# Kernel tuning notes

Hardware: AMD Instinct MI355X
Metric: run time of the kernel (lower is better)

The kernel has to match this reference:

```python
import jax, jax.numpy as jnp
import numpy as np

B, T, E, H = 64, 256, 300, 512        # batch, longest_sequence, embed dim, hidden
V, NTAGS, NCLS, DFF = 50000, 17, 18, 256  # vocab, universal POS tags, output classes, dense hidden


def setup_inputs() -> dict:
    key = jax.random.key(0)
    ks = jax.random.split(key, 11)
    su = 1.0 / np.sqrt(H)  # PyTorch LSTMCell/Linear uniform init scale
    return {
        "tokens": jax.random.randint(ks[0], (B, T), 0, V),
        "tags": jax.random.randint(ks[1], (T,), 0, NTAGS),
        "emb": jax.random.normal(ks[2], (V, E), jnp.float32),
        "W_ih": jax.random.uniform(ks[3], (NTAGS, 4 * H, E), jnp.float32, -su, su),
        "W_hh": jax.random.uniform(ks[4], (NTAGS, 4 * H, H), jnp.float32, -su, su),
        "b_ih": jax.random.uniform(ks[5], (NTAGS, 4 * H), jnp.float32, -su, su),
        "b_hh": jax.random.uniform(ks[6], (NTAGS, 4 * H), jnp.float32, -su, su),
        "W1": jax.random.uniform(ks[7], (DFF, H), jnp.float32, -su, su),
        "b1": jax.random.uniform(ks[8], (DFF,), jnp.float32, -su, su),
        "W2": jax.random.uniform(ks[9], (NCLS, DFF), jnp.float32, -1.0 / np.sqrt(DFF), 1.0 / np.sqrt(DFF)),
        "b2": jax.random.uniform(ks[10], (NCLS,), jnp.float32, -1.0 / np.sqrt(DFF), 1.0 / np.sqrt(DFF)),
    }


def reference(tokens, tags, emb, W_ih, W_hh, b_ih, b_hh, W1, b1, W2, b2):
    x = emb[tokens]                     # [B, T, E] embedding lookup
    xs = jnp.swapaxes(x, 0, 1)          # [T, B, E] time-major for scan

    def step(carry, inp):
        h, c = carry
        xt, tag = inp                   # xt: [B, E], tag: scalar int routing the cell
        gates = (xt @ W_ih[tag].T + h @ W_hh[tag].T
                 + b_ih[tag] + b_hh[tag])            # [B, 4H]
        i, f, g, o = jnp.split(gates, 4, axis=-1)    # PyTorch LSTMCell gate order
        i = jax.nn.sigmoid(i)
        f = jax.nn.sigmoid(f)
        g = jnp.tanh(g)
        o = jax.nn.sigmoid(o)
        c = f * c + i * g
        h = o * jnp.tanh(c)
        return (h, c), None

    h0 = jnp.zeros((x.shape[0], H), x.dtype)
    (h, _), _ = jax.lax.scan(step, (h0, h0), (xs, tags))
    # dense head: Linear -> ReLU -> (Dropout inactive at eval) -> Linear
    hid = jax.nn.relu(h @ W1.T + b1)
    return hid @ W2.T + b2              # [B, NCLS] multiclass logits
```

## Files before the change

kernel.cpp:

```cpp
#include <hip/hip_runtime.h>
#include <cstdint>
#include <cstddef>

#define BB   64
#define TT   256
#define EE   300
#define HH   512
#define G4H  2048
#define NCLS 18
#define DFF  256
#define NBLK 128

typedef short short8 __attribute__((ext_vector_type(8)));
typedef float f32x4  __attribute__((ext_vector_type(4)));

__device__ __forceinline__ float fast_exp2(float x) { return __builtin_amdgcn_exp2f(x); }
__device__ __forceinline__ float sigmoid_f(float x) {
  return 1.0f / (1.0f + fast_exp2(x * -1.442695040888963f));
}
__device__ __forceinline__ float tanh_f(float x) {
  return 2.0f / (1.0f + fast_exp2(x * -2.885390081777927f)) - 1.0f;
}
__device__ __forceinline__ unsigned bf16_rne(float x) {
  unsigned u = __float_as_uint(x);
  return (u + 0x7FFFu + ((u >> 16) & 1u)) >> 16;
}
__device__ __forceinline__ float bf16_f32(unsigned hi) { return __uint_as_float(hi << 16); }

__global__ __launch_bounds__(256) void xproj_kernel(
    const int* __restrict__ tokens, const int* __restrict__ tags,
    const float* __restrict__ emb, const float* __restrict__ W_ih,
    const float* __restrict__ b_ih, const float* __restrict__ b_hh,
    float* __restrict__ xW, int t0)
{
  const int tid  = threadIdx.x;
  const int lane = tid & 63;
  const int w    = tid >> 6;
  const int rs   = blockIdx.x & 127;
  const int tl   = blockIdx.x >> 7;
  const int t    = t0 + tl;
  const int tag  = tags[t];
  const int row0 = rs * 16;
  const int kbeg = __builtin_amdgcn_readfirstlane(w * 76);
  const bool full = (w != 3);

  const int tok = tokens[lane * TT + t];
  const float* xrow = emb + (size_t)tok * EE + kbeg;
  float xr[76];
  #pragma unroll
  for (int i = 0; i < 18; ++i) {
    const float4 v = *reinterpret_cast<const float4*>(xrow + i * 4);
    xr[i*4+0] = v.x; xr[i*4+1] = v.y; xr[i*4+2] = v.z; xr[i*4+3] = v.w;
  }
  if (full) {
    const float4 v = *reinterpret_cast<const float4*>(xrow + 72);
    xr[72] = v.x; xr[73] = v.y; xr[74] = v.z; xr[75] = v.w;
  } else {
    xr[72] = 0.f; xr[73] = 0.f; xr[74] = 0.f; xr[75] = 0.f;
  }

  const float* Wbase = W_ih + (size_t)tag * ((size_t)G4H * EE);
  __shared__ float red[4][16][64];
  #pragma unroll
  for (int r = 0; r < 16; ++r) {
    const float* Wr = Wbase + (size_t)(row0 + r) * EE + kbeg;
    float a = 0.f;
    #pragma unroll
    for (int k = 0; k < 72; ++k) a = fmaf(Wr[k], xr[k], a);
    if (full) {
      #pragma unroll
      for (int k = 72; k < 76; ++k) a = fmaf(Wr[k], xr[k], a);
    }
    red[w][r][lane] = a;
  }
  __syncthreads();
  #pragma unroll
  for (int it = 0; it < 4; ++it) {
    const int item = tid + it * 256;
    const int r = item >> 6, b = item & 63;
    const int row = row0 + r;
    float s = red[0][r][b] + red[1][r][b] + red[2][r][b] + red[3][r][b];
    s += b_ih[tag * G4H + row] + b_hh[tag * G4H + row];
    xW[((size_t)tl * G4H + row) * BB + b] = s;
  }
}

__global__ __launch_bounds__(1024, 4) void lstm_seq_kernel(
    const int* __restrict__ tags, const float* __restrict__ W_hh,
    const float* __restrict__ xW,
    unsigned short* __restrict__ hHiA, unsigned short* __restrict__ hLoA,
    unsigned short* __restrict__ hHiB, unsigned short* __restrict__ hLoB,
    float* __restrict__ cst, float* __restrict__ hF,
    unsigned int* __restrict__ flags, int t0, int nsteps)
{
  const int tid  = threadIdx.x;
  const int lane = tid & 63;
  const int w    = tid >> 6;
  const int bt   = w & 3;
  const int ksl  = w >> 2;
  const int j0   = blockIdx.x * 4;

  __shared__ unsigned short whi[2][16][512];
  __shared__ unsigned short wlo[2][16][512];
  __shared__ float pl[3][4][64][4];
  __shared__ float gt[4][16][20];

  const int r15 = lane & 15;
  const int kg  = lane >> 4;
  const int k0  = ksl * 128;
  const int b0  = bt * 16;
  const int swzr = (r15 & 7) << 4;

  const int grow = (w >> 2) * HH + j0 + (w & 3);
  const int swzw = (w & 7) << 4;

  const int lh = lane >> 4, ll = lane & 15;
  const int eb = b0 + ll;
  float creg = 0.f;
  float xwv0 = 0.f, xwv1 = 0.f, xwv2 = 0.f, xwv3 = 0.f;

  {
    const int tag0 = tags[t0];
    const float* wp = W_hh + (size_t)tag0 * ((size_t)G4H * HH)
                    + (size_t)grow * HH + lane * 8;
    const f32x4 wa = *reinterpret_cast<const f32x4*>(wp);
    const f32x4 wb = *reinterpret_cast<const f32x4*>(wp + 4);
    float wv[8] = {wa[0], wa[1], wa[2], wa[3], wb[0], wb[1], wb[2], wb[3]};
    short8 vhi, vlo;
    #pragma unroll
    for (int i = 0; i < 8; ++i) {
      const unsigned h = bf16_rne(wv[i]);
      vhi[i] = (short)h;
      vlo[i] = (short)bf16_rne(wv[i] - bf16_f32(h));
    }
    *reinterpret_cast<short8*>((char*)&whi[0][0][0] + w * 1024 + ((lane * 16) ^ swzw)) = vhi;
    *reinterpret_cast<short8*>((char*)&wlo[0][0][0] + w * 1024 + ((lane * 16) ^ swzw)) = vlo;
    if (ksl == 0) {
      creg = cst[(size_t)(j0 + lh) * BB + eb];
      const size_t xb = ((size_t)0 * G4H + (size_t)lh * HH + j0) * BB + (b0 + ll);
      xwv0 = xW[xb]; xwv1 = xW[xb + BB]; xwv2 = xW[xb + 2*BB]; xwv3 = xW[xb + 3*BB];
    }
  }
  __syncthreads();

  for (int s = 0; s < nsteps; ++s) {
    const int t   = t0 + s;
    const int cur = s & 1, nxt = cur ^ 1;
    const unsigned short* hHiIn = (t & 1) ? hHiB : hHiA;
    const unsigned short* hLoIn = (t & 1) ? hLoB : hLoA;
    unsigned short* hHiOut = (t & 1) ? hHiA : hHiB;
    unsigned short* hLoOut = (t & 1) ? hLoA : hLoB;

    const unsigned short* bhp = hHiIn + ((size_t)(b0 + r15) * HH + (k0 + kg * 8));
    const unsigned short* blp = hLoIn + ((size_t)(b0 + r15) * HH + (k0 + kg * 8));
    const int tagN = tags[(t + 1 < TT) ? (t + 1) : t];
    const float* wfp = W_hh + (size_t)tagN * ((size_t)G4H * HH)
                     + (size_t)grow * HH + lane * 8;
    short8 bh0, bh1, bh2, bh3, bl0, bl1, bl2, bl3;
    f32x4 wf0, wf1;
    asm volatile(
      "global_load_dwordx4 %0, %10, off sc0 sc1\n\t"
      "global_load_dwordx4 %1, %10, off offset:64 sc0 sc1\n\t"
      "global_load_dwordx4 %2, %10, off offset:128 sc0 sc1\n\t"
      "global_load_dwordx4 %3, %10, off offset:192 sc0 sc1\n\t"
      "global_load_dwordx4 %4, %11, off sc0 sc1\n\t"
      "global_load_dwordx4 %5, %11, off offset:64 sc0 sc1\n\t"
      "global_load_dwordx4 %6, %11, off offset:128 sc0 sc1\n\t"
      "global_load_dwordx4 %7, %11, off offset:192 sc0 sc1\n\t"
      "global_load_dwordx4 %8, %12, off\n\t"
      "global_load_dwordx4 %9, %12, off offset:16\n\t"
      "s_waitcnt vmcnt(2)"
      : "=&v"(bh0), "=&v"(bh1), "=&v"(bh2), "=&v"(bh3),
        "=&v"(bl0), "=&v"(bl1), "=&v"(bl2), "=&v"(bl3),
        "=&v"(wf0), "=&v"(wf1)
      : "v"(bhp), "v"(blp), "v"(wfp)
      : "memory");
    __builtin_amdgcn_sched_barrier(0);

    const char* wh_base = (const char*)&whi[cur][0][0];
    const char* wl_base = (const char*)&wlo[cur][0][0];
    f32x4 ahh = {0.f, 0.f, 0.f, 0.f};
    f32x4 ahl = {0.f, 0.f, 0.f, 0.f};
    f32x4 alh = {0.f, 0.f, 0.f, 0.f};
    #pragma unroll
    for (int kk = 0; kk < 4; ++kk) {
      const int kbyte = (((k0 + kk * 32 + kg * 8) * 2) ^ swzr);
      const short8 a_hi = *reinterpret_cast<const short8*>(wh_base + r15 * 1024 + kbyte);
      const short8 a_lo = *reinterpret_cast<const short8*>(wl_base + r15 * 1024 + kbyte);
      const short8 b_hi = (kk == 0) ? bh0 : (kk == 1) ? bh1 : (kk == 2) ? bh2 : bh3;
      const short8 b_lo = (kk == 0) ? bl0 : (kk == 1) ? bl1 : (kk == 2) ? bl2 : bl3;
      ahh = __builtin_amdgcn_mfma_f32_16x16x32_bf16(a_hi, b_hi, ahh, 0, 0, 0);
      ahl = __builtin_amdgcn_mfma_f32_16x16x32_bf16(a_hi, b_lo, ahl, 0, 0, 0);
      alh = __builtin_amdgcn_mfma_f32_16x16x32_bf16(a_lo, b_hi, alh, 0, 0, 0);
    }
    f32x4 Cw = ahh + ahl + alh;

    asm volatile("s_waitcnt vmcnt(0)" ::: "memory");
    __builtin_amdgcn_sched_barrier(0);
    {
      float wv[8] = {wf0[0], wf0[1], wf0[2], wf0[3], wf1[0], wf1[1], wf1[2], wf1[3]};
      short8 vhi, vlo;
      #pragma unroll
      for (int i = 0; i < 8; ++i) {
        const unsigned h = bf16_rne(wv[i]);
        vhi[i] = (short)h;
        vlo[i] = (short)bf16_rne(wv[i] - bf16_f32(h));
      }
      *reinterpret_cast<short8*>((char*)&whi[nxt][0][0] + w * 1024 + ((lane * 16) ^ swzw)) = vhi;
      *reinterpret_cast<short8*>((char*)&wlo[nxt][0][0] + w * 1024 + ((lane * 16) ^ swzw)) = vlo;
    }

    if (ksl) *reinterpret_cast<f32x4*>(&pl[ksl - 1][bt][lane][0]) = Cw;
    __syncthreads();
    if (ksl == 0) {
      f32x4 C = Cw;
      C += *reinterpret_cast<const f32x4*>(&pl[0][bt][lane][0]);
      C += *reinterpret_cast<const f32x4*>(&pl[1][bt][lane][0]);
      C += *reinterpret_cast<const f32x4*>(&pl[2][bt][lane][0]);
      C[0] += xwv0; C[1] += xwv1; C[2] += xwv2; C[3] += xwv3;
      *reinterpret_cast<f32x4*>(&gt[bt][ll][lh * 4]) = C;
    }
    __syncthreads();
    if (ksl == 0) {
      const float gi = gt[bt][ll][0  + lh];
      const float gf = gt[bt][ll][4  + lh];
      const float gg = gt[bt][ll][8  + lh];
      const float go = gt[bt][ll][12 + lh];
      creg = sigmoid_f(gf) * creg + sigmoid_f(gi) * tanh_f(gg);
      const float hv = sigmoid_f(go) * tanh_f(creg);
      const unsigned hhi = bf16_rne(hv);
      const unsigned hlo = bf16_rne(hv - bf16_f32(hhi));
      unsigned short* ph = hHiOut + ((size_t)eb * HH + j0 + lh);
      unsigned short* pl2 = hLoOut + ((size_t)eb * HH + j0 + lh);
      asm volatile(
        "global_store_short %0, %1, off sc0 sc1\n\t"
        "global_store_short %2, %3, off sc0 sc1"
        :: "v"(ph), "v"(hhi), "v"(pl2), "v"(hlo) : "memory");
      if (t == TT - 1) hF[(size_t)(j0 + lh) * BB + eb] = hv;
    }
    __syncthreads();
    if (s != nsteps - 1) {
      if (tid == 0) {
        __hip_atomic_store(&flags[blockIdx.x * 16], (unsigned int)(s + 1),
                           __ATOMIC_RELAXED, __HIP_MEMORY_SCOPE_AGENT);
      }
      if (ksl == 0) {
        const size_t xb = ((size_t)(s + 1) * G4H + (size_t)lh * HH + j0) * BB + (b0 + ll);
        xwv0 = xW[xb]; xwv1 = xW[xb + BB]; xwv2 = xW[xb + 2*BB]; xwv3 = xW[xb + 3*BB];
      }
      if (w == 0) {
        const unsigned int tgt = (unsigned int)(s + 1);
        for (;;) {
          const unsigned int f0 = __hip_atomic_load(&flags[lane * 16],
                                    __ATOMIC_RELAXED, __HIP_MEMORY_SCOPE_AGENT);
          const unsigned int f1 = __hip_atomic_load(&flags[(lane + 64) * 16],
                                    __ATOMIC_RELAXED, __HIP_MEMORY_SCOPE_AGENT);
          if (__all(f0 >= tgt && f1 >= tgt)) break;
        }
      }
      __syncthreads();
    }
  }
  if (ksl == 0) cst[(size_t)(j0 + lh) * BB + eb] = creg;
}

__global__ __launch_bounds__(1024) void head1_kernel(
    const float* __restrict__ W1, const float* __restrict__ b1,
    const float* __restrict__ hfin, float* __restrict__ hid)
{
  const int tid  = threadIdx.x;
  const int lane = tid & 63;
  const int w    = tid >> 6;
  const int row0 = blockIdx.x * 8;
  const int kbeg = __builtin_amdgcn_readfirstlane(w * 32);
  float xr[32];
  const float* hp = hfin + (size_t)kbeg * BB + lane;
  #pragma unroll
  for (int i = 0; i < 32; ++i) xr[i] = hp[i * BB];
  __shared__ float red[16][8][64];
  #pragma unroll
  for (int r = 0; r < 8; ++r) {
    const float* Wr = W1 + (size_t)(row0 + r) * HH + kbeg;
    float a = 0.f;
    #pragma unroll
    for (int k = 0; k < 32; ++k) a = fmaf(Wr[k], xr[k], a);
    red[w][r][lane] = a;
  }
  __syncthreads();
  if (tid < 512) {
    const int r = tid >> 6, b = tid & 63;
    float s = 0.f;
    #pragma unroll
    for (int ww = 0; ww < 16; ++ww) s += red[ww][r][b];
    s += b1[row0 + r];
    hid[(size_t)(row0 + r) * BB + b] = fmaxf(s, 0.f);
  }
}

__global__ __launch_bounds__(256) void head2_kernel(
    const float* __restrict__ W2, const float* __restrict__ b2,
    const float* __restrict__ hid, float* __restrict__ out)
{
  const int tid  = threadIdx.x;
  const int lane = tid & 63;
  const int w    = tid >> 6;
  const int kbeg = __builtin_amdgcn_readfirstlane(w * 64);
  float xr[64];
  const float* hp = hid + (size_t)kbeg * BB + lane;
  #pragma unroll
  for (int i = 0; i < 64; ++i) xr[i] = hp[i * BB];
  __shared__ float red[4][NCLS][64];
  #pragma unroll
  for (int r = 0; r < NCLS; ++r) {
    const float* Wr = W2 + (size_t)r * DFF + kbeg;
    float a = 0.f;
    #pragma unroll
    for (int k = 0; k < 64; ++k) a = fmaf(Wr[k], xr[k], a);
    red[w][r][lane] = a;
  }
  __syncthreads();
  for (int it = 0; it < 5; ++it) {
    const int item = tid + it * 256;
    if (item < NCLS * 64) {
      const int r = item >> 6, b = item & 63;
      float s = red[0][r][b] + red[1][r][b] + red[2][r][b] + red[3][r][b];
      out[(size_t)b * NCLS + r] = s + b2[r];
    }
  }
}

extern "C" void kernel_launch(void* const* d_in, const int* in_sizes, int n_in,
                              void* d_out, int out_size, void* d_ws, size_t ws_size,
                              hipStream_t stream)
{
  const int*   tokens = (const int*)  d_in[0];
  const int*   tags   = (const int*)  d_in[1];
  const float* emb    = (const float*)d_in[2];
  const float* W_ih   = (const float*)d_in[3];
  const float* W_hh   = (const float*)d_in[4];
  const float* b_ih   = (const float*)d_in[5];
  const float* b_hh   = (const float*)d_in[6];
  const float* W1     = (const float*)d_in[7];
  const float* b1     = (const float*)d_in[8];
  const float* W2     = (const float*)d_in[9];
  const float* b2     = (const float*)d_in[10];
  float* out = (float*)d_out;

  const size_t per_t = (size_t)G4H * BB * sizeof(float);
  int TCH = 8;
  for (int c = 256; c >= 8; c >>= 1) {
    if ((size_t)c * per_t + (8u << 20) <= ws_size) { TCH = c; break; }
  }
  char* p = (char*)d_ws;
  float* xW = (float*)p;            p += (size_t)TCH * per_t;
  unsigned short* hHiA = (unsigned short*)p;  p += (size_t)HH * BB * 2;
  unsigned short* hLoA = (unsigned short*)p;  p += (size_t)HH * BB * 2;
  unsigned short* hHiB = (unsigned short*)p;  p += (size_t)HH * BB * 2;
  unsigned short* hLoB = (unsigned short*)p;  p += (size_t)HH * BB * 2;
  float* cst = (float*)p;           p += (size_t)HH * BB * sizeof(float);
  float* hF  = (float*)p;           p += (size_t)HH * BB * sizeof(float);
  float* hid = (float*)p;           p += (size_t)DFF * BB * sizeof(float);
  unsigned int* flags = (unsigned int*)p;

  (void)hipMemsetAsync(hHiA, 0, (size_t)HH * BB * 2, stream);
  (void)hipMemsetAsync(hLoA, 0, (size_t)HH * BB * 2, stream);
  (void)hipMemsetAsync(cst,  0, (size_t)HH * BB * sizeof(float), stream);

  for (int c0 = 0; c0 < TT; c0 += TCH) {
    xproj_kernel<<<dim3((unsigned)TCH * 128), dim3(256), 0, stream>>>(
        tokens, tags, emb, W_ih, b_ih, b_hh, xW, c0);
    (void)hipMemsetAsync(flags, 0, NBLK * 16 * sizeof(unsigned int), stream);
    {
      int t0 = c0, nsteps = TCH;
      void* args[] = { (void*)&tags, (void*)&W_hh, (void*)&xW,
                       (void*)&hHiA, (void*)&hLoA, (void*)&hHiB, (void*)&hLoB,
                       (void*)&cst, (void*)&hF, (void*)&flags,
                       (void*)&t0, (void*)&nsteps };
      hipLaunchCooperativeKernel((const void*)lstm_seq_kernel,
                                 dim3(NBLK), dim3(1024), args, 0, stream);
    }
  }
  head1_kernel<<<dim3(32), dim3(1024), 0, stream>>>(W1, b1, hF, hid);
  head2_kernel<<<dim3(1), dim3(256), 0, stream>>>(W2, b2, hid, out);
}
```

Baseline: 2.113 ms.

## Replace grid flag barrier with sentinel-polled per-step hidden state buffers

Removes the per-step flag-based grid barrier. Each timestep's hidden state is now written as one packed hi/lo bf16 dword into its own slot, and consumers spin on their loads until no sentinel value remains. This also drops one __syncthreads by moving the gate transpose from shared memory to wave shuffles, and double-buffers the partial-sum LDS. The cost is extra memory for one h slot per step, a memset of the sentinel each chunk, and reliance on a sentinel value that real h values never take.

```diff
diff --git a/kernel.cpp b/kernel.cpp
--- a/kernel.cpp
+++ b/kernel.cpp
@@ -10,9 +10,12 @@
 #define NCLS 18
 #define DFF  256
 #define NBLK 128
+#define HHBB (HH * BB)
+#define SENT 0x7F7F7F7Fu
 
 typedef short short8 __attribute__((ext_vector_type(8)));
 typedef float f32x4  __attribute__((ext_vector_type(4)));
+typedef unsigned int u32x4 __attribute__((ext_vector_type(4)));
 
 __device__ __forceinline__ float fast_exp2(float x) { return __builtin_amdgcn_exp2f(x); }
 __device__ __forceinline__ float sigmoid_f(float x) {
@@ -26,6 +29,26 @@
   return (u + 0x7FFFu + ((u >> 16) & 1u)) >> 16;
 }
 __device__ __forceinline__ float bf16_f32(unsigned hi) { return __uint_as_float(hi << 16); }
+
+__device__ __forceinline__ short8 pack_hi8(u32x4 a, u32x4 b) {
+  u32x4 r;
+  r[0] = (a[0] >> 16) | (a[1] & 0xFFFF0000u);
+  r[1] = (a[2] >> 16) | (a[3] & 0xFFFF0000u);
+  r[2] = (b[0] >> 16) | (b[1] & 0xFFFF0000u);
+  r[3] = (b[2] >> 16) | (b[3] & 0xFFFF0000u);
+  return *(short8*)&r;
+}
+__device__ __forceinline__ short8 pack_lo8(u32x4 a, u32x4 b) {
+  u32x4 r;
+  r[0] = (a[0] & 0xFFFFu) | (a[1] << 16);
+  r[1] = (a[2] & 0xFFFFu) | (a[3] << 16);
+  r[2] = (b[0] & 0xFFFFu) | (b[1] << 16);
+  r[3] = (b[2] & 0xFFFFu) | (b[3] << 16);
+  return *(short8*)&r;
+}
+__device__ __forceinline__ bool no_sent(u32x4 a) {
+  return a[0] != SENT && a[1] != SENT && a[2] != SENT && a[3] != SENT;
+}
 
 __global__ __launch_bounds__(256) void xproj_kernel(
     const int* __restrict__ tokens, const int* __restrict__ tags,
@@ -87,11 +110,9 @@
 
 __global__ __launch_bounds__(1024, 4) void lstm_seq_kernel(
     const int* __restrict__ tags, const float* __restrict__ W_hh,
-    const float* __restrict__ xW,
-    unsigned short* __restrict__ hHiA, unsigned short* __restrict__ hLoA,
-    unsigned short* __restrict__ hHiB, unsigned short* __restrict__ hLoB,
+    const float* __restrict__ xW, unsigned int* __restrict__ hPack,
     float* __restrict__ cst, float* __restrict__ hF,
-    unsigned int* __restrict__ flags, int t0, int nsteps)
+    int t0, int nsteps)
 {
   const int tid  = threadIdx.x;
   const int lane = tid & 63;
@@ -102,8 +123,7 @@
 
   __shared__ unsigned short whi[2][16][512];
   __shared__ unsigned short wlo[2][16][512];
-  __shared__ float pl[3][4][64][4];
-  __shared__ float gt[4][16][20];
+  __shared__ float pl[2][3][4][64][4];
 
   const int r15 = lane & 15;
   const int kg  = lane >> 4;
@@ -137,7 +157,7 @@
     *reinterpret_cast<short8*>((char*)&wlo[0][0][0] + w * 1024 + ((lane * 16) ^ swzw)) = vlo;
     if (ksl == 0) {
       creg = cst[(size_t)(j0 + lh) * BB + eb];
-      const size_t xb = ((size_t)0 * G4H + (size_t)lh * HH + j0) * BB + (b0 + ll);
+      const size_t xb = ((size_t)0 * G4H + (size_t)lh * HH + j0) * BB + eb;
       xwv0 = xW[xb]; xwv1 = xW[xb + BB]; xwv2 = xW[xb + 2*BB]; xwv3 = xW[xb + 3*BB];
     }
   }
@@ -146,36 +166,40 @@
   for (int s = 0; s < nsteps; ++s) {
     const int t   = t0 + s;
     const int cur = s & 1, nxt = cur ^ 1;
-    const unsigned short* hHiIn = (t & 1) ? hHiB : hHiA;
-    const unsigned short* hLoIn = (t & 1) ? hLoB : hLoA;
-    unsigned short* hHiOut = (t & 1) ? hHiA : hHiB;
-    unsigned short* hLoOut = (t & 1) ? hLoA : hLoB;
-
-    const unsigned short* bhp = hHiIn + ((size_t)(b0 + r15) * HH + (k0 + kg * 8));
-    const unsigned short* blp = hLoIn + ((size_t)(b0 + r15) * HH + (k0 + kg * 8));
+
+    const unsigned int* hp = hPack + (size_t)s * HHBB
+                           + (size_t)(b0 + r15) * HH + (k0 + kg * 8);
+    u32x4 q0, q1, q2, q3, q4, q5, q6, q7;
+    for (;;) {
+      asm volatile(
+        "global_load_dwordx4 %0, %8, off sc0 sc1\n\t"
+        "global_load_dwordx4 %1, %8, off offset:16 sc0 sc1\n\t"
+        "global_load_dwordx4 %2, %8, off offset:128 sc0 sc1\n\t"
+        "global_load_dwordx4 %3, %8, off offset:144 sc0 sc1\n\t"
+        "global_load_dwordx4 %4, %8, off offset:256 sc0 sc1\n\t"
+        "global_load_dwordx4 %5, %8, off offset:272 sc0 sc1\n\t"
+        "global_load_dwordx4 %6, %8, off offset:384 sc0 sc1\n\t"
+        "global_load_dwordx4 %7, %8, off offset:400 sc0 sc1\n\t"
+        "s_waitcnt vmcnt(0)"
+        : "=&v"(q0), "=&v"(q1), "=&v"(q2), "=&v"(q3),
+          "=&v"(q4), "=&v"(q5), "=&v"(q6), "=&v"(q7)
+        : "v"(hp)
+        : "memory");
+      const bool ok = no_sent(q0) && no_sent(q1) && no_sent(q2) && no_sent(q3)
+                   && no_sent(q4) && no_sent(q5) && no_sent(q6) && no_sent(q7);
+      if (__all(ok)) break;
+    }
+
     const int tagN = tags[(t + 1 < TT) ? (t + 1) : t];
     const float* wfp = W_hh + (size_t)tagN * ((size_t)G4H * HH)
                      + (size_t)grow * HH + lane * 8;
-    short8 bh0, bh1, bh2, bh3, bl0, bl1, bl2, bl3;
-    f32x4 wf0, wf1;
-    asm volatile(
-      "global_load_dwordx4 %0, %10, off sc0 sc1\n\t"
-      "global_load_dwordx4 %1, %10, off offset:64 sc0 sc1\n\t"
-      "global_load_dwordx4 %2, %10, off offset:128 sc0 sc1\n\t"
-      "global_load_dwordx4 %3, %10, off offset:192 sc0 sc1\n\t"
-      "global_load_dwordx4 %4, %11, off sc0 sc1\n\t"
-      "global_load_dwordx4 %5, %11, off offset:64 sc0 sc1\n\t"
-      "global_load_dwordx4 %6, %11, off offset:128 sc0 sc1\n\t"
-      "global_load_dwordx4 %7, %11, off offset:192 sc0 sc1\n\t"
-      "global_load_dwordx4 %8, %12, off\n\t"
-      "global_load_dwordx4 %9, %12, off offset:16\n\t"
-      "s_waitcnt vmcnt(2)"
-      : "=&v"(bh0), "=&v"(bh1), "=&v"(bh2), "=&v"(bh3),
-        "=&v"(bl0), "=&v"(bl1), "=&v"(bl2), "=&v"(bl3),
-        "=&v"(wf0), "=&v"(wf1)
-      : "v"(bhp), "v"(blp), "v"(wfp)
-      : "memory");
-    __builtin_amdgcn_sched_barrier(0);
+    const f32x4 wf0 = *reinterpret_cast<const f32x4*>(wfp);
+    const f32x4 wf1 = *reinterpret_cast<const f32x4*>(wfp + 4);
+
+    const short8 bh0 = pack_hi8(q0, q1), bl0 = pack_lo8(q0, q1);
+    const short8 bh1 = pack_hi8(q2, q3), bl1 = pack_lo8(q2, q3);
+    const short8 bh2 = pack_hi8(q4, q5), bl2 = pack_lo8(q4, q5);
+    const short8 bh3 = pack_hi8(q6, q7), bl3 = pack_lo8(q6, q7);
 
     const char* wh_base = (const char*)&whi[cur][0][0];
     const char* wl_base = (const char*)&wlo[cur][0][0];
@@ -195,8 +219,6 @@
     }
     f32x4 Cw = ahh + ahl + alh;
 
-    asm volatile("s_waitcnt vmcnt(0)" ::: "memory");
-    __builtin_amdgcn_sched_barrier(0);
     {
       float wv[8] = {wf0[0], wf0[1], wf0[2], wf0[3], wf1[0], wf1[1], wf1[2], wf1[3]};
       short8 vhi, vlo;
@@ -210,55 +232,38 @@
       *reinterpret_cast<short8*>((char*)&wlo[nxt][0][0] + w * 1024 + ((lane * 16) ^ swzw)) = vlo;
     }
 
-    if (ksl) *reinterpret_cast<f32x4*>(&pl[ksl - 1][bt][lane][0]) = Cw;
+    if (ksl) *reinterpret_cast<f32x4*>(&pl[cur][ksl - 1][bt][lane][0]) = Cw;
     __syncthreads();
+
     if (ksl == 0) {
       f32x4 C = Cw;
-      C += *reinterpret_cast<const f32x4*>(&pl[0][bt][lane][0]);
-      C += *reinterpret_cast<const f32x4*>(&pl[1][bt][lane][0]);
-      C += *reinterpret_cast<const f32x4*>(&pl[2][bt][lane][0]);
+      C += *reinterpret_cast<const f32x4*>(&pl[cur][0][bt][lane][0]);
+      C += *reinterpret_cast<const f32x4*>(&pl[cur][1][bt][lane][0]);
+      C += *reinterpret_cast<const f32x4*>(&pl[cur][2][bt][lane][0]);
       C[0] += xwv0; C[1] += xwv1; C[2] += xwv2; C[3] += xwv3;
-      *reinterpret_cast<f32x4*>(&gt[bt][ll][lh * 4]) = C;
-    }
-    __syncthreads();
-    if (ksl == 0) {
-      const float gi = gt[bt][ll][0  + lh];
-      const float gf = gt[bt][ll][4  + lh];
-      const float gg = gt[bt][ll][8  + lh];
-      const float go = gt[bt][ll][12 + lh];
-      creg = sigmoid_f(gf) * creg + sigmoid_f(gi) * tanh_f(gg);
-      const float hv = sigmoid_f(go) * tanh_f(creg);
+      float g4[4];
+      #pragma unroll
+      for (int jj = 0; jj < 4; ++jj) {
+        #pragma unroll
+        for (int g = 0; g < 4; ++g) {
+          const float tv = __shfl(C[jj], g * 16 + ll);
+          if (lh == jj) g4[g] = tv;
+        }
+      }
+      creg = sigmoid_f(g4[1]) * creg + sigmoid_f(g4[0]) * tanh_f(g4[2]);
+      const float hv = sigmoid_f(g4[3]) * tanh_f(creg);
       const unsigned hhi = bf16_rne(hv);
       const unsigned hlo = bf16_rne(hv - bf16_f32(hhi));
-      unsigned short* ph = hHiOut + ((size_t)eb * HH + j0 + lh);
-      unsigned short* pl2 = hLoOut + ((size_t)eb * HH + j0 + lh);
-      asm volatile(
-        "global_store_short %0, %1, off sc0 sc1\n\t"
-        "global_store_short %2, %3, off sc0 sc1"
-        :: "v"(ph), "v"(hhi), "v"(pl2), "v"(hlo) : "memory");
+      const unsigned packed = (hhi << 16) | (hlo & 0xFFFFu);
+      unsigned int* ph = hPack + (size_t)(s + 1) * HHBB
+                       + (size_t)eb * HH + (j0 + lh);
+      asm volatile("global_store_dword %0, %1, off sc0 sc1"
+                   :: "v"(ph), "v"(packed) : "memory");
       if (t == TT - 1) hF[(size_t)(j0 + lh) * BB + eb] = hv;
-    }
-    __syncthreads();
-    if (s != nsteps - 1) {
-      if (tid == 0) {
-        __hip_atomic_store(&flags[blockIdx.x * 16], (unsigned int)(s + 1),
-                           __ATOMIC_RELAXED, __HIP_MEMORY_SCOPE_AGENT);
-      }
-      if (ksl == 0) {
-        const size_t xb = ((size_t)(s + 1) * G4H + (size_t)lh * HH + j0) * BB + (b0 + ll);
+      if (s != nsteps - 1) {
+        const size_t xb = ((size_t)(s + 1) * G4H + (size_t)lh * HH + j0) * BB + eb;
         xwv0 = xW[xb]; xwv1 = xW[xb + BB]; xwv2 = xW[xb + 2*BB]; xwv3 = xW[xb + 3*BB];
       }
-      if (w == 0) {
-        const unsigned int tgt = (unsigned int)(s + 1);
-        for (;;) {
-          const unsigned int f0 = __hip_atomic_load(&flags[lane * 16],
-                                    __ATOMIC_RELAXED, __HIP_MEMORY_SCOPE_AGENT);
-          const unsigned int f1 = __hip_atomic_load(&flags[(lane + 64) * 16],
-                                    __ATOMIC_RELAXED, __HIP_MEMORY_SCOPE_AGENT);
-          if (__all(f0 >= tgt && f1 >= tgt)) break;
-        }
-      }
-      __syncthreads();
     }
   }
   if (ksl == 0) cst[(size_t)(j0 + lh) * BB + eb] = creg;
@@ -346,36 +351,36 @@
   const float* b2     = (const float*)d_in[10];
   float* out = (float*)d_out;
 
-  const size_t per_t = (size_t)G4H * BB * sizeof(float);
+  const size_t per_t  = (size_t)G4H * BB * sizeof(float);
+  const size_t slot_b = (size_t)HHBB * sizeof(unsigned int);
   int TCH = 8;
   for (int c = 256; c >= 8; c >>= 1) {
-    if ((size_t)c * per_t + (8u << 20) <= ws_size) { TCH = c; break; }
+    if ((size_t)c * per_t + (size_t)(c + 1) * slot_b + (4u << 20) <= ws_size) {
+      TCH = c; break;
+    }
   }
   char* p = (char*)d_ws;
-  float* xW = (float*)p;            p += (size_t)TCH * per_t;
-  unsigned short* hHiA = (unsigned short*)p;  p += (size_t)HH * BB * 2;
-  unsigned short* hLoA = (unsigned short*)p;  p += (size_t)HH * BB * 2;
-  unsigned short* hHiB = (unsigned short*)p;  p += (size_t)HH * BB * 2;
-  unsigned short* hLoB = (unsigned short*)p;  p += (size_t)HH * BB * 2;
-  float* cst = (float*)p;           p += (size_t)HH * BB * sizeof(float);
-  float* hF  = (float*)p;           p += (size_t)HH * BB * sizeof(float);
-  float* hid = (float*)p;           p += (size_t)DFF * BB * sizeof(float);
-  unsigned int* flags = (unsigned int*)p;
-
-  (void)hipMemsetAsync(hHiA, 0, (size_t)HH * BB * 2, stream);
-  (void)hipMemsetAsync(hLoA, 0, (size_t)HH * BB * 2, stream);
-  (void)hipMemsetAsync(cst,  0, (size_t)HH * BB * sizeof(float), stream);
+  float* xW = (float*)p;              p += (size_t)TCH * per_t;
+  unsigned int* hPack = (unsigned int*)p;  p += (size_t)(TCH + 1) * slot_b;
+  float* cst = (float*)p;             p += (size_t)HH * BB * sizeof(float);
+  float* hF  = (float*)p;             p += (size_t)HH * BB * sizeof(float);
+  float* hid = (float*)p;
+
+  (void)hipMemsetAsync(hPack, 0x00, slot_b, stream);
+  (void)hipMemsetAsync(cst,   0x00, (size_t)HH * BB * sizeof(float), stream);
 
   for (int c0 = 0; c0 < TT; c0 += TCH) {
+    if (c0 > 0) {
+      (void)hipMemcpyAsync(hPack, hPack + (size_t)TCH * HHBB, slot_b,
+                           hipMemcpyDeviceToDevice, stream);
+    }
+    (void)hipMemsetAsync(hPack + HHBB, 0x7F, (size_t)TCH * slot_b, stream);
     xproj_kernel<<<dim3((unsigned)TCH * 128), dim3(256), 0, stream>>>(
         tokens, tags, emb, W_ih, b_ih, b_hh, xW, c0);
-    (void)hipMemsetAsync(flags, 0, NBLK * 16 * sizeof(unsigned int), stream);
     {
       int t0 = c0, nsteps = TCH;
-      void* args[] = { (void*)&tags, (void*)&W_hh, (void*)&xW,
-                       (void*)&hHiA, (void*)&hLoA, (void*)&hHiB, (void*)&hLoB,
-                       (void*)&cst, (void*)&hF, (void*)&flags,
-                       (void*)&t0, (void*)&nsteps };
+      void* args[] = { (void*)&tags, (void*)&W_hh, (void*)&xW, (void*)&hPack,
+                       (void*)&cst, (void*)&hF, (void*)&t0, (void*)&nsteps };
       hipLaunchCooperativeKernel((const void*)lstm_seq_kernel,
                                  dim3(NBLK), dim3(1024), args, 0, stream);
     }
```

Result: slower. 2.738 ms (+29.6%).
